# Kernel optimization log

Hardware: AMD Instinct MI355X
Metric: run time of the kernel (lower is better)

## Reference

```python
import jax, jax.numpy as jnp
import numpy as np

N = 4096   # n_roi
E = 131072 # edges (avg degree 32)
B = 64     # batch of subjects/windows sharing one connectome
K = 4      # Chebyshev order


def _cheb_params(key, cin, cout):
    kw, kb = jax.random.split(key)
    w = jax.random.normal(kw, (K, cin, cout), dtype=jnp.float32) / np.sqrt(K * cin)
    b = jax.random.normal(kb, (cout,), dtype=jnp.float32) * 0.01
    return w, b


def _lin_params(key, cin, cout):
    kw, kb = jax.random.split(key)
    w = jax.random.normal(kw, (cin, cout), dtype=jnp.float32) / np.sqrt(cin)
    b = jax.random.normal(kb, (cout,), dtype=jnp.float32) * 0.01
    return w, b


def setup_inputs() -> dict:
    key = jax.random.key(0)
    ks = jax.random.split(key, 12)
    x = jax.random.normal(ks[0], (B, N, 1), dtype=jnp.float32)
    src = jax.random.randint(ks[1], (E,), 0, N, dtype=jnp.int32)
    dst = jax.random.randint(ks[2], (E,), 0, N, dtype=jnp.int32)
    edge_weight = jax.random.uniform(ks[3], (E,), dtype=jnp.float32)
    w1, b1 = _cheb_params(ks[4], 1, 32)
    w2, b2 = _cheb_params(ks[5], 32, 32)
    w3, b3 = _cheb_params(ks[6], 32, 32)
    w4, b4 = _cheb_params(ks[7], 32, 32)
    w5, b5 = _cheb_params(ks[8], 32, 4)
    fw1, fb1 = _lin_params(ks[9], N * 4, 128)
    fw2, fb2 = _lin_params(ks[10], 128, 128)
    fw3, fb3 = _lin_params(ks[11], 128, 9)
    return dict(x=x, src=src, dst=dst, edge_weight=edge_weight,
                w1=w1, b1=b1, w2=w2, b2=b2, w3=w3, b3=b3,
                w4=w4, b4=b4, w5=w5, b5=b5,
                fw1=fw1, fb1=fb1, fw2=fw2, fb2=fb2, fw3=fw3, fb3=fb3)


def _norm_weights(src, dst, edge_weight):
    # PyG ChebConv default: sym normalization, lambda_max=2 ->
    # L_hat = -D^{-1/2} A D^{-1/2}, diagonal 2/lambda_max - 1 = 0 (self-loop skipped)
    deg = jax.ops.segment_sum(edge_weight, src, num_segments=N)
    dinv = jnp.where(deg > 0, jax.lax.rsqrt(jnp.maximum(deg, 1e-30)), 0.0)
    return -dinv[src] * edge_weight * dinv[dst]


def _propagate(z, src, dst, nw):
    # z: [B, N, C] -> L_hat @ z  via gather-multiply-scatter over edges
    msg = nw[None, :, None] * z[:, src, :]          # [B, E, C]
    msg = jnp.swapaxes(msg, 0, 1)                    # [E, B, C]
    agg = jax.ops.segment_sum(msg, dst, num_segments=N)  # [N, B, C]
    return jnp.swapaxes(agg, 0, 1)                   # [B, N, C]


def _cheb_conv(x, src, dst, nw, w, b):
    # x: [B,N,Cin], w: [K,Cin,Cout]
    tx0 = x
    out = jnp.einsum('bni,io->bno', tx0, w[0])
    tx1 = _propagate(tx0, src, dst, nw)
    out = out + jnp.einsum('bni,io->bno', tx1, w[1])
    for k in range(2, K):
        tx2 = 2.0 * _propagate(tx1, src, dst, nw) - tx0
        out = out + jnp.einsum('bni,io->bno', tx2, w[k])
        tx0, tx1 = tx1, tx2
    return out + b


def reference(x, src, dst, edge_weight, w1, b1, w2, b2, w3, b3, w4, b4, w5, b5,
              fw1, fb1, fw2, fb2, fw3, fb3):
    nw = _norm_weights(src, dst, edge_weight)
    h = jax.nn.relu(_cheb_conv(x, src, dst, nw, w1, b1))
    h = jax.nn.relu(_cheb_conv(h, src, dst, nw, w2, b2))
    h = jax.nn.relu(_cheb_conv(h, src, dst, nw, w3, b3))
    h = jax.nn.relu(_cheb_conv(h, src, dst, nw, w4, b4))
    h = jax.nn.relu(_cheb_conv(h, src, dst, nw, w5, b5))  # [B, N, 4]
    h = h.reshape(B, N * 4)
    # original has dropout (identity at eval) and NO relu between fc layers
    h = h @ fw1 + fb1
    h = h @ fw2 + fb2
    return h @ fw3 + fb3  # [B, 9]
```

## Files before the change

### kernel.cpp

```cpp
#include <hip/hip_runtime.h>
#include <cstdint>

#define NN 4096
#define EE 131072
#define BB 64
#define EPAD (EE + 8 * NN)

typedef float f4 __attribute__((ext_vector_type(4)));
typedef unsigned short ushort_t;
typedef unsigned int uint_t;

__device__ __forceinline__ f4 up4(uint2 u) {
    f4 r;
    r.x = __uint_as_float(u.x << 16);
    r.y = __uint_as_float(u.x & 0xffff0000u);
    r.z = __uint_as_float(u.y << 16);
    r.w = __uint_as_float(u.y & 0xffff0000u);
    return r;
}
__device__ __forceinline__ void up8(uint4 u, f4& lo, f4& hi) {
    lo.x = __uint_as_float(u.x << 16);
    lo.y = __uint_as_float(u.x & 0xffff0000u);
    lo.z = __uint_as_float(u.y << 16);
    lo.w = __uint_as_float(u.y & 0xffff0000u);
    hi.x = __uint_as_float(u.z << 16);
    hi.y = __uint_as_float(u.z & 0xffff0000u);
    hi.z = __uint_as_float(u.w << 16);
    hi.w = __uint_as_float(u.w & 0xffff0000u);
}
__device__ __forceinline__ uint_t bfpk(float a, float b) {
    uint_t xa = __float_as_uint(a); xa = (xa + 0x7fffu + ((xa >> 16) & 1u)) >> 16;
    uint_t xb = __float_as_uint(b); xb = (xb + 0x7fffu + ((xb >> 16) & 1u));
    return (xa & 0xffffu) | (xb & 0xffff0000u);
}

__global__ void k_deg_hist(const int* __restrict__ src, const int* __restrict__ dst,
                           const float* __restrict__ ew, float* __restrict__ deg,
                           int* __restrict__ cnt) {
    int e = blockIdx.x * blockDim.x + threadIdx.x;
    if (e >= EE) return;
    atomicAdd(&deg[src[e]], ew[e]);
    atomicAdd(&cnt[dst[e]], 1);
}

__global__ __launch_bounds__(1024) void k_scan(const int* __restrict__ cnt,
                                               int* __restrict__ rowptr,
                                               int* __restrict__ cursor) {
    __shared__ int s[1024];
    int tid = threadIdx.x;
    int p0 = (cnt[tid * 4 + 0] + 7) & ~7;
    int p1 = (cnt[tid * 4 + 1] + 7) & ~7;
    int p2 = (cnt[tid * 4 + 2] + 7) & ~7;
    int p3 = (cnt[tid * 4 + 3] + 7) & ~7;
    int sum = p0 + p1 + p2 + p3;
    s[tid] = sum;
    __syncthreads();
    for (int off = 1; off < 1024; off <<= 1) {
        int t = (tid >= off) ? s[tid - off] : 0;
        __syncthreads();
        s[tid] += t;
        __syncthreads();
    }
    int excl = s[tid] - sum;
    rowptr[tid * 4 + 0] = excl; cursor[tid * 4 + 0] = excl; excl += p0;
    rowptr[tid * 4 + 1] = excl; cursor[tid * 4 + 1] = excl; excl += p1;
    rowptr[tid * 4 + 2] = excl; cursor[tid * 4 + 2] = excl; excl += p2;
    rowptr[tid * 4 + 3] = excl; cursor[tid * 4 + 3] = excl; excl += p3;
    if (tid == 1023) rowptr[4096] = excl;
}

__global__ void k_fill(const int* __restrict__ src, const int* __restrict__ dst,
                       const float* __restrict__ ew, const float* __restrict__ deg,
                       int* __restrict__ cursor, int2* __restrict__ cv) {
    int e = blockIdx.x * blockDim.x + threadIdx.x;
    if (e >= EE) return;
    int s = src[e], d = dst[e];
    int pos = atomicAdd(&cursor[d], 1);
    float ds = deg[s], dd = deg[d];
    float is = ds > 0.f ? rsqrtf(fmaxf(ds, 1e-30f)) : 0.f;
    float id = dd > 0.f ? rsqrtf(fmaxf(dd, 1e-30f)) : 0.f;
    float v = -(is * ew[e] * id);
    cv[pos] = make_int2(s, __float_as_int(v));
}

__global__ __launch_bounds__(256) void k_transpose_x(const float* __restrict__ x,
                                                     float* __restrict__ X0) {
    __shared__ float s[64 * 65];
    int n0 = blockIdx.x * 64;
    for (int idx = threadIdx.x; idx < 4096; idx += 256) {
        int b = idx >> 6, nl = idx & 63;
        s[nl * 65 + b] = x[(size_t)b * NN + n0 + nl];
    }
    __syncthreads();
    for (int idx = threadIdx.x; idx < 4096; idx += 256) {
        int nl = idx >> 6, b = idx & 63;
        X0[(size_t)(n0 + nl) * 64 + b] = s[nl * 65 + b];
    }
}

__global__ __launch_bounds__(64) void k_spmm_narrow(const int* __restrict__ rowptr,
                                                    const int2* __restrict__ cv,
                                                    const float* __restrict__ Zin,
                                                    const float* __restrict__ Tprev,
                                                    float* __restrict__ Tout,
                                                    float alpha, int useprev) {
    int n = blockIdx.x;
    int lane = threadIdx.x;
    int start = rowptr[n], end = rowptr[n + 1];
    float acc = 0.f;
    for (int e = start; e < end; e += 8) {
        const int4* q = reinterpret_cast<const int4*>(cv + e);
        int4 a = q[0], b = q[1], c = q[2], d = q[3];
        float z0 = Zin[((size_t)a.x << 6) + lane];
        float z1 = Zin[((size_t)a.z << 6) + lane];
        float z2 = Zin[((size_t)b.x << 6) + lane];
        float z3 = Zin[((size_t)b.z << 6) + lane];
        float z4 = Zin[((size_t)c.x << 6) + lane];
        float z5 = Zin[((size_t)c.z << 6) + lane];
        float z6 = Zin[((size_t)d.x << 6) + lane];
        float z7 = Zin[((size_t)d.z << 6) + lane];
        acc += __int_as_float(a.y) * z0 + __int_as_float(a.w) * z1
             + __int_as_float(b.y) * z2 + __int_as_float(b.w) * z3
             + __int_as_float(c.y) * z4 + __int_as_float(c.w) * z5
             + __int_as_float(d.y) * z6 + __int_as_float(d.w) * z7;
    }
    size_t o = ((size_t)n << 6) + lane;
    float r = alpha * acc;
    if (useprev) r -= Tprev[o];
    Tout[o] = r;
}

__global__ __launch_bounds__(256) void k_expand1(const float* __restrict__ T0,
                                                 const float* __restrict__ T1,
                                                 const float* __restrict__ T2,
                                                 const float* __restrict__ T3,
                                                 const float* __restrict__ w1,
                                                 const float* __restrict__ b1,
                                                 ushort_t* __restrict__ H) {
    __shared__ float sT[4][64];
    __shared__ float sW[128];
    __shared__ float sB[32];
    int n = blockIdx.x, tid = threadIdx.x;
    {
        int k = tid >> 6, b = tid & 63;
        const float* Tk = (k == 0) ? T0 : (k == 1) ? T1 : (k == 2) ? T2 : T3;
        sT[k][b] = Tk[(size_t)n * 64 + b];
    }
    if (tid < 128) sW[tid] = w1[tid];
    if (tid < 32) sB[tid] = b1[tid];
    __syncthreads();
    int col0 = tid * 8;
    int b = tid >> 2;
    int co0 = col0 & 31;
    float t0 = sT[0][b], t1 = sT[1][b], t2 = sT[2][b], t3 = sT[3][b];
    float r[8];
#pragma unroll
    for (int j = 0; j < 8; ++j) {
        int co = co0 + j;
        float v = t0 * sW[co] + t1 * sW[32 + co] + t2 * sW[64 + co] + t3 * sW[96 + co] + sB[co];
        r[j] = v > 0.f ? v : 0.f;
    }
    uint4 st;
    st.x = bfpk(r[0], r[1]); st.y = bfpk(r[2], r[3]);
    st.z = bfpk(r[4], r[5]); st.w = bfpk(r[6], r[7]);
    *reinterpret_cast<uint4*>(H + (size_t)n * 2048 + col0) = st;
}

__global__ __launch_bounds__(256) void k_spmm_pure(const int* __restrict__ rowptr,
                                                   const int2* __restrict__ cv,
                                                   const ushort_t* __restrict__ Zg,
                                                   const ushort_t* __restrict__ Pown,
                                                   ushort_t* __restrict__ Tout) {
    int chunk = blockIdx.x & 3;
    int rowblk = blockIdx.x >> 2;
    int wave = threadIdx.x >> 6;
    int lane = threadIdx.x & 63;
    int n = rowblk * 4 + wave;
    int col0 = chunk * 512 + lane * 8;

    int start = rowptr[n], end = rowptr[n + 1];
    f4 aL0 = {0,0,0,0}, aH0 = {0,0,0,0}, aL1 = {0,0,0,0}, aH1 = {0,0,0,0};
    for (int e = start; e < end; e += 8) {
        const int4* q = reinterpret_cast<const int4*>(cv + e);
        int4 a = q[0], b = q[1], c = q[2], d = q[3];
        uint4 u0 = *reinterpret_cast<const uint4*>(Zg + (((size_t)a.x) << 11) + col0);
        uint4 u1 = *reinterpret_cast<const uint4*>(Zg + (((size_t)a.z) << 11) + col0);
        uint4 u2 = *reinterpret_cast<const uint4*>(Zg + (((size_t)b.x) << 11) + col0);
        uint4 u3 = *reinterpret_cast<const uint4*>(Zg + (((size_t)b.z) << 11) + col0);
        uint4 u4 = *reinterpret_cast<const uint4*>(Zg + (((size_t)c.x) << 11) + col0);
        uint4 u5 = *reinterpret_cast<const uint4*>(Zg + (((size_t)c.z) << 11) + col0);
        uint4 u6 = *reinterpret_cast<const uint4*>(Zg + (((size_t)d.x) << 11) + col0);
        uint4 u7 = *reinterpret_cast<const uint4*>(Zg + (((size_t)d.z) << 11) + col0);
        f4 lo, hi;
        up8(u0, lo, hi); aL0 += __int_as_float(a.y) * lo; aH0 += __int_as_float(a.y) * hi;
        up8(u1, lo, hi); aL1 += __int_as_float(a.w) * lo; aH1 += __int_as_float(a.w) * hi;
        up8(u2, lo, hi); aL0 += __int_as_float(b.y) * lo; aH0 += __int_as_float(b.y) * hi;
        up8(u3, lo, hi); aL1 += __int_as_float(b.w) * lo; aH1 += __int_as_float(b.w) * hi;
        up8(u4, lo, hi); aL0 += __int_as_float(c.y) * lo; aH0 += __int_as_float(c.y) * hi;
        up8(u5, lo, hi); aL1 += __int_as_float(c.w) * lo; aH1 += __int_as_float(c.w) * hi;
        up8(u6, lo, hi); aL0 += __int_as_float(d.y) * lo; aH0 += __int_as_float(d.y) * hi;
        up8(u7, lo, hi); aL1 += __int_as_float(d.w) * lo; aH1 += __int_as_float(d.w) * hi;
    }
    size_t o = (((size_t)n) << 11) + col0;
    f4 tL = aL0 + aL1, tH = aH0 + aH1;
    if (Pown) {
        uint4 pu = *reinterpret_cast<const uint4*>(Pown + o);
        f4 pL, pH;
        up8(pu, pL, pH);
        tL = 2.f * tL - pL;
        tH = 2.f * tH - pH;
    }
    uint4 st;
    st.x = bfpk(tL.x, tL.y); st.y = bfpk(tL.z, tL.w);
    st.z = bfpk(tH.x, tH.y); st.w = bfpk(tH.z, tH.w);
    *reinterpret_cast<uint4*>(Tout + o) = st;
}

template <int COUT, bool OUTBF>
__global__ __launch_bounds__(256, 4) void k_cheb_out(
    const int* __restrict__ rowptr, const int2* __restrict__ cv,
    const ushort_t* __restrict__ T2g,
    const ushort_t* __restrict__ T1,
    const ushort_t* __restrict__ H,
    const float* __restrict__ W,
    const float* __restrict__ bias,
    void* __restrict__ OUTv)
{
    __shared__ float sW[4 * 32 * COUT];
    __shared__ uint_t sPu[4][4][320];

    int chunk = blockIdx.x & 3;
    int rowblk = blockIdx.x >> 2;
    int wave = threadIdx.x >> 6;
    int lane = threadIdx.x & 63;
    int n = rowblk * 4 + wave;
    int col0 = chunk * 512 + lane * 8;
    int tid = threadIdx.x;

    for (int idx = tid; idx < 4 * 32 * COUT; idx += 256) sW[idx] = W[idx];

    int start = rowptr[n], end = rowptr[n + 1];
    f4 aL0 = {0,0,0,0}, aH0 = {0,0,0,0}, aL1 = {0,0,0,0}, aH1 = {0,0,0,0};
    for (int e = start; e < end; e += 8) {
        const int4* q = reinterpret_cast<const int4*>(cv + e);
        int4 a = q[0], b = q[1], c = q[2], d = q[3];
        uint4 u0 = *reinterpret_cast<const uint4*>(T2g + (((size_t)a.x) << 11) + col0);
        uint4 u1 = *reinterpret_cast<const uint4*>(T2g + (((size_t)a.z) << 11) + col0);
        uint4 u2 = *reinterpret_cast<const uint4*>(T2g + (((size_t)b.x) << 11) + col0);
        uint4 u3 = *reinterpret_cast<const uint4*>(T2g + (((size_t)b.z) << 11) + col0);
        uint4 u4 = *reinterpret_cast<const uint4*>(T2g + (((size_t)c.x) << 11) + col0);
        uint4 u5 = *reinterpret_cast<const uint4*>(T2g + (((size_t)c.z) << 11) + col0);
        uint4 u6 = *reinterpret_cast<const uint4*>(T2g + (((size_t)d.x) << 11) + col0);
        uint4 u7 = *reinterpret_cast<const uint4*>(T2g + (((size_t)d.z) << 11) + col0);
        f4 lo, hi;
        up8(u0, lo, hi); aL0 += __int_as_float(a.y) * lo; aH0 += __int_as_float(a.y) * hi;
        up8(u1, lo, hi); aL1 += __int_as_float(a.w) * lo; aH1 += __int_as_float(a.w) * hi;
        up8(u2, lo, hi); aL0 += __int_as_float(b.y) * lo; aH0 += __int_as_float(b.y) * hi;
        up8(u3, lo, hi); aL1 += __int_as_float(b.w) * lo; aH1 += __int_as_float(b.w) * hi;
        up8(u4, lo, hi); aL0 += __int_as_float(c.y) * lo; aH0 += __int_as_float(c.y) * hi;
        up8(u5, lo, hi); aL1 += __int_as_float(c.w) * lo; aH1 += __int_as_float(c.w) * hi;
        up8(u6, lo, hi); aL0 += __int_as_float(d.y) * lo; aH0 += __int_as_float(d.y) * hi;
        up8(u7, lo, hi); aL1 += __int_as_float(d.w) * lo; aH1 += __int_as_float(d.w) * hi;
    }
    size_t o = (((size_t)n) << 11) + col0;

    int g = lane >> 2, qd = lane & 3;
    int si = g * 20 + qd * 4;
    {
        uint4 pu = *reinterpret_cast<const uint4*>(T1 + o);
        f4 pL, pH;
        up8(pu, pL, pH);
        f4 tL = 2.f * (aL0 + aL1) - pL;
        f4 tH = 2.f * (aH0 + aH1) - pH;
        uint4 st;
        st.x = bfpk(tL.x, tL.y); st.y = bfpk(tL.z, tL.w);
        st.z = bfpk(tH.x, tH.y); st.w = bfpk(tH.z, tH.w);
        *reinterpret_cast<uint4*>(&sPu[wave][3][si]) = st;
        *reinterpret_cast<uint4*>(&sPu[wave][1][si]) = pu;
    }
    *reinterpret_cast<uint4*>(&sPu[wave][2][si]) =
        *reinterpret_cast<const uint4*>(T2g + o);
    *reinterpret_cast<uint4*>(&sPu[wave][0][si]) =
        *reinterpret_cast<const uint4*>(H + o);
    __syncthreads();

    if constexpr (COUT == 32) {
        int co0 = qd * 8;
        f4 oacc0 = {0,0,0,0}, oacc1 = {0,0,0,0};
#pragma unroll
        for (int u = 0; u < 16; ++u) {
#pragma unroll
            for (int p = 0; p < 4; ++p) {
                uint_t au = sPu[wave][p][g * 20 + u];
                float alo = __uint_as_float(au << 16);
                float ahi = __uint_as_float(au & 0xffff0000u);
                const float* wr0 = &sW[p * 1024 + (2 * u) * 32 + co0];
                const float* wr1 = &sW[p * 1024 + (2 * u + 1) * 32 + co0];
                oacc0 += alo * *reinterpret_cast<const f4*>(wr0);
                oacc1 += alo * *reinterpret_cast<const f4*>(wr0 + 4);
                oacc0 += ahi * *reinterpret_cast<const f4*>(wr1);
                oacc1 += ahi * *reinterpret_cast<const f4*>(wr1 + 4);
            }
        }
        f4 r0, r1;
        r0.x = oacc0.x + bias[co0 + 0]; r0.y = oacc0.y + bias[co0 + 1];
        r0.z = oacc0.z + bias[co0 + 2]; r0.w = oacc0.w + bias[co0 + 3];
        r1.x = oacc1.x + bias[co0 + 4]; r1.y = oacc1.y + bias[co0 + 5];
        r1.z = oacc1.z + bias[co0 + 6]; r1.w = oacc1.w + bias[co0 + 7];
        r0.x = r0.x > 0.f ? r0.x : 0.f; r0.y = r0.y > 0.f ? r0.y : 0.f;
        r0.z = r0.z > 0.f ? r0.z : 0.f; r0.w = r0.w > 0.f ? r0.w : 0.f;
        r1.x = r1.x > 0.f ? r1.x : 0.f; r1.y = r1.y > 0.f ? r1.y : 0.f;
        r1.z = r1.z > 0.f ? r1.z : 0.f; r1.w = r1.w > 0.f ? r1.w : 0.f;
        if constexpr (OUTBF) {
            uint4 st;
            st.x = bfpk(r0.x, r0.y); st.y = bfpk(r0.z, r0.w);
            st.z = bfpk(r1.x, r1.y); st.w = bfpk(r1.z, r1.w);
            *reinterpret_cast<uint4*>((ushort_t*)OUTv + o) = st;
        } else {
            float* po = (float*)OUTv + o;
            *reinterpret_cast<f4*>(po) = r0;
            *reinterpret_cast<f4*>(po + 4) = r1;
        }
    } else {
        int co = lane & 3;
        float o0 = 0.f;
#pragma unroll
        for (int u = 0; u < 16; ++u) {
#pragma unroll
            for (int p = 0; p < 4; ++p) {
                uint_t au = sPu[wave][p][g * 20 + u];
                float alo = __uint_as_float(au << 16);
                float ahi = __uint_as_float(au & 0xffff0000u);
                o0 += alo * sW[p * 128 + (2 * u) * 4 + co]
                    + ahi * sW[p * 128 + (2 * u + 1) * 4 + co];
            }
        }
        float r = o0 + bias[co];
        r = r > 0.f ? r : 0.f;
        ((float*)OUTv)[n * 256 + chunk * 64 + lane] = r;
    }
}

__global__ __launch_bounds__(256) void k_fc1(const float* __restrict__ H5,
                                             const float* __restrict__ fw1,
                                             float* __restrict__ fc1out) {
    __shared__ float hT[128 * 65];
    __shared__ float wS[32 * 128];
    int tid = threadIdx.x;
    int n0 = blockIdx.x * 32;
    for (int idx = tid; idx < 8192; idx += 256) {
        int n_l = idx >> 8;
        int rem = idx & 255;
        int b = rem >> 2, c = rem & 3;
        int kk = n_l * 4 + c;
        hT[kk * 65 + b] = H5[(size_t)(n0 + n_l) * 256 + rem];
    }
    float acc[8][4];
#pragma unroll
    for (int i = 0; i < 8; ++i)
#pragma unroll
        for (int j = 0; j < 4; ++j) acc[i][j] = 0.f;
    int bq = tid >> 5;
    int jq = tid & 31;
    for (int kb = 0; kb < 128; kb += 32) {
        __syncthreads();
        for (int idx = tid; idx < 4096; idx += 256) {
            int kl = idx >> 7, j = idx & 127;
            wS[idx] = fw1[(size_t)(n0 * 4 + kb + kl) * 128 + j];
        }
        __syncthreads();
        for (int kl = 0; kl < 32; ++kl) {
            int kk = kb + kl;
            float4 w = *reinterpret_cast<const float4*>(&wS[kl * 128 + jq * 4]);
#pragma unroll
            for (int bi = 0; bi < 8; ++bi) {
                float h = hT[kk * 65 + bq * 8 + bi];
                acc[bi][0] += h * w.x;
                acc[bi][1] += h * w.y;
                acc[bi][2] += h * w.z;
                acc[bi][3] += h * w.w;
            }
        }
    }
#pragma unroll
    for (int bi = 0; bi < 8; ++bi)
#pragma unroll
        for (int ji = 0; ji < 4; ++ji)
            atomicAdd(&fc1out[(bq * 8 + bi) * 128 + jq * 4 + ji], acc[bi][ji]);
}

__global__ __launch_bounds__(128) void k_fc23(const float* __restrict__ fc1out,
                                              const float* __restrict__ fb1,
                                              const float* __restrict__ fw2,
                                              const float* __restrict__ fb2,
                                              const float* __restrict__ fw3,
                                              const float* __restrict__ fb3,
                                              float* __restrict__ out) {
    int b = blockIdx.x;
    int j = threadIdx.x;
    __shared__ float r[128];
    __shared__ float s1[128];
    r[j] = fc1out[b * 128 + j] + fb1[j];
    __syncthreads();
    float acc = fb2[j];
    for (int i = 0; i < 128; ++i) acc += r[i] * fw2[i * 128 + j];
    s1[j] = acc;
    __syncthreads();
    if (j < 9) {
        float a2 = fb3[j];
        for (int i = 0; i < 128; ++i) a2 += s1[i] * fw3[i * 9 + j];
        out[b * 9 + j] = a2;
    }
}

extern "C" void kernel_launch(void* const* d_in, const int* in_sizes, int n_in,
                              void* d_out, int out_size, void* d_ws, size_t ws_size,
                              hipStream_t stream) {
    const float* x   = (const float*)d_in[0];
    const int*   src = (const int*)d_in[1];
    const int*   dst = (const int*)d_in[2];
    const float* ew  = (const float*)d_in[3];
    const float* w1  = (const float*)d_in[4];
    const float* b1  = (const float*)d_in[5];
    const float* w2  = (const float*)d_in[6];
    const float* b2  = (const float*)d_in[7];
    const float* w3  = (const float*)d_in[8];
    const float* b3  = (const float*)d_in[9];
    const float* w4  = (const float*)d_in[10];
    const float* b4  = (const float*)d_in[11];
    const float* w5  = (const float*)d_in[12];
    const float* b5  = (const float*)d_in[13];
    const float* fw1 = (const float*)d_in[14];
    const float* fb1 = (const float*)d_in[15];
    const float* fw2 = (const float*)d_in[16];
    const float* fb2 = (const float*)d_in[17];
    const float* fw3 = (const float*)d_in[18];
    const float* fb3 = (const float*)d_in[19];
    float* out = (float*)d_out;

    char* p = (char*)d_ws;
    const size_t XBYTES = (size_t)NN * 2048 * 2;
    ushort_t* X0 = (ushort_t*)(p + 0 * XBYTES);
    ushort_t* X1 = (ushort_t*)(p + 1 * XBYTES);
    ushort_t* X2 = (ushort_t*)(p + 2 * XBYTES);
    ushort_t* X3 = (ushort_t*)(p + 3 * XBYTES);
    size_t off = 4 * XBYTES;
    float* H5     = (float*)(p + off); off += (size_t)NN * 256 * 4;
    float* deg    = (float*)(p + off); off += (size_t)NN * 4;
    int*   cnt    = (int*)(p + off);   off += (size_t)NN * 4;
    int*   cursor = (int*)(p + off);   off += (size_t)NN * 4;
    int*   rowptr = (int*)(p + off);   off += (size_t)(NN + 4) * 4;
    int2*  cv     = (int2*)(p + off);  off += (size_t)EPAD * 8;
    float* fc1o   = (float*)(p + off); off += (size_t)BB * 128 * 4;
    float* xn0    = (float*)(p + off); off += (size_t)NN * 64 * 4;
    float* tn1    = (float*)(p + off); off += (size_t)NN * 64 * 4;
    float* tn2    = (float*)(p + off); off += (size_t)NN * 64 * 4;
    float* tn3    = (float*)(p + off); off += (size_t)NN * 64 * 4;
    if (off > ws_size) return;

    hipMemsetAsync(deg, 0, NN * 4, stream);
    hipMemsetAsync(cnt, 0, NN * 4, stream);
    hipMemsetAsync(cv, 0, (size_t)EPAD * 8, stream);
    hipMemsetAsync(fc1o, 0, BB * 128 * 4, stream);

    k_deg_hist<<<EE / 256, 256, 0, stream>>>(src, dst, ew, deg, cnt);
    k_scan<<<1, 1024, 0, stream>>>(cnt, rowptr, cursor);
    k_fill<<<EE / 256, 256, 0, stream>>>(src, dst, ew, deg, cursor, cv);
    k_transpose_x<<<NN / 64, 256, 0, stream>>>(x, xn0);

    k_spmm_narrow<<<NN, 64, 0, stream>>>(rowptr, cv, xn0, nullptr, tn1, 1.f, 0);
    k_spmm_narrow<<<NN, 64, 0, stream>>>(rowptr, cv, tn1, xn0, tn2, 2.f, 1);
    k_spmm_narrow<<<NN, 64, 0, stream>>>(rowptr, cv, tn2, tn1, tn3, 2.f, 1);
    k_expand1<<<NN, 256, 0, stream>>>(xn0, tn1, tn2, tn3, w1, b1, X3);

    const int GRID4 = (NN / 4) * 4;
    auto run32 = [&](const ushort_t* H, ushort_t* T1, ushort_t* T2, ushort_t* OUT,
                     const float* W, const float* B) {
        k_spmm_pure<<<GRID4, 256, 0, stream>>>(rowptr, cv, H, nullptr, T1);
        k_spmm_pure<<<GRID4, 256, 0, stream>>>(rowptr, cv, T1, H, T2);
        k_cheb_out<32, true><<<GRID4, 256, 0, stream>>>(rowptr, cv, T2, T1, H, W, B, OUT);
    };
    run32(X3, X0, X1, X2, w2, b2);
    run32(X2, X3, X0, X1, w3, b3);
    run32(X1, X2, X3, X0, w4, b4);

    k_spmm_pure<<<GRID4, 256, 0, stream>>>(rowptr, cv, X0, nullptr, X1);
    k_spmm_pure<<<GRID4, 256, 0, stream>>>(rowptr, cv, X1, X0, X2);
    k_cheb_out<4, false><<<GRID4, 256, 0, stream>>>(rowptr, cv, X2, X1, X0, w5, b5, H5);

    k_fc1<<<128, 256, 0, stream>>>(H5, fw1, fc1o);
    k_fc23<<<BB, 128, 0, stream>>>(fc1o, fb1, fw2, fb2, fw3, fb3, out);
}
```

Measured before the change: 644.1 us.

## Use bf16 MFMA for the Chebyshev output projection in cheb_out kernel

Replaces the scalar FP32 FMA loop that projects the four Chebyshev terms (128 inputs to 32 outputs per node/batch slice) with bf16 MFMA 16x16x32 instructions. The weights are converted to packed bf16 in shared memory in a transposed layout so they can serve as B fragments. Launch bounds are raised to 5 blocks per CU. The change drops weight precision to bf16 and writes the output as scattered 16-bit stores instead of vectorized ones. The COUT==32 path now always writes bf16, ignoring the OUTBF template flag.

```diff
diff --git a/kernel.cpp b/kernel.cpp
--- a/kernel.cpp
+++ b/kernel.cpp
@@ -7,17 +7,10 @@
 #define EPAD (EE + 8 * NN)
 
 typedef float f4 __attribute__((ext_vector_type(4)));
+typedef short bf16x8 __attribute__((ext_vector_type(8)));
 typedef unsigned short ushort_t;
 typedef unsigned int uint_t;
 
-__device__ __forceinline__ f4 up4(uint2 u) {
-    f4 r;
-    r.x = __uint_as_float(u.x << 16);
-    r.y = __uint_as_float(u.x & 0xffff0000u);
-    r.z = __uint_as_float(u.y << 16);
-    r.w = __uint_as_float(u.y & 0xffff0000u);
-    return r;
-}
 __device__ __forceinline__ void up8(uint4 u, f4& lo, f4& hi) {
     lo.x = __uint_as_float(u.x << 16);
     lo.y = __uint_as_float(u.x & 0xffff0000u);
@@ -32,6 +25,10 @@
     uint_t xa = __float_as_uint(a); xa = (xa + 0x7fffu + ((xa >> 16) & 1u)) >> 16;
     uint_t xb = __float_as_uint(b); xb = (xb + 0x7fffu + ((xb >> 16) & 1u));
     return (xa & 0xffffu) | (xb & 0xffff0000u);
+}
+__device__ __forceinline__ ushort_t bf1(float a) {
+    uint_t x = __float_as_uint(a);
+    return (ushort_t)((x + 0x7fffu + ((x >> 16) & 1u)) >> 16);
 }
 
 __global__ void k_deg_hist(const int* __restrict__ src, const int* __restrict__ dst,
@@ -217,7 +214,7 @@
 }
 
 template <int COUT, bool OUTBF>
-__global__ __launch_bounds__(256, 4) void k_cheb_out(
+__global__ __launch_bounds__(256, 5) void k_cheb_out(
     const int* __restrict__ rowptr, const int2* __restrict__ cv,
     const ushort_t* __restrict__ T2g,
     const ushort_t* __restrict__ T1,
@@ -226,8 +223,9 @@
     const float* __restrict__ bias,
     void* __restrict__ OUTv)
 {
-    __shared__ float sW[4 * 32 * COUT];
     __shared__ uint_t sPu[4][4][320];
+    __shared__ uint_t sWb[(COUT == 32) ? 2560 : 1];
+    __shared__ float  sWf[(COUT == 4) ? 512 : 1];
 
     int chunk = blockIdx.x & 3;
     int rowblk = blockIdx.x >> 2;
@@ -237,7 +235,16 @@
     int col0 = chunk * 512 + lane * 8;
     int tid = threadIdx.x;
 
-    for (int idx = tid; idx < 4 * 32 * COUT; idx += 256) sW[idx] = W[idx];
+    if constexpr (COUT == 32) {
+        for (int idx = tid; idx < 2048; idx += 256) {
+            int p = idx >> 9, rem = idx & 511;
+            int co = rem >> 4, u = rem & 15;
+            sWb[p * 640 + co * 20 + u] =
+                bfpk(W[p * 1024 + (2 * u) * 32 + co], W[p * 1024 + (2 * u + 1) * 32 + co]);
+        }
+    } else {
+        for (int idx = tid; idx < 4 * 32 * COUT; idx += 256) sWf[idx] = W[idx];
+    }
 
     int start = rowptr[n], end = rowptr[n + 1];
     f4 aL0 = {0,0,0,0}, aH0 = {0,0,0,0}, aL1 = {0,0,0,0}, aH1 = {0,0,0,0};
@@ -285,8 +292,34 @@
     __syncthreads();
 
     if constexpr (COUT == 32) {
-        int co0 = qd * 8;
-        f4 oacc0 = {0,0,0,0}, oacc1 = {0,0,0,0};
+        int mr = lane & 15;
+        int qk = lane >> 4;
+        f4 accA = {0,0,0,0}, accB = {0,0,0,0};
+#pragma unroll
+        for (int kk = 0; kk < 4; ++kk) {
+            bf16x8 af = *reinterpret_cast<const bf16x8*>(&sPu[wave][kk][mr * 20 + qk * 4]);
+            bf16x8 b0 = *reinterpret_cast<const bf16x8*>(&sWb[kk * 640 + mr * 20 + qk * 4]);
+            bf16x8 b1 = *reinterpret_cast<const bf16x8*>(&sWb[kk * 640 + (16 + mr) * 20 + qk * 4]);
+            accA = __builtin_amdgcn_mfma_f32_16x16x32_bf16(af, b0, accA, 0, 0, 0);
+            accB = __builtin_amdgcn_mfma_f32_16x16x32_bf16(af, b1, accB, 0, 0, 0);
+        }
+        int co = lane & 15;
+        float bA = bias[co], bB = bias[co + 16];
+        ushort_t* OB = (ushort_t*)OUTv;
+        size_t obase = (((size_t)n) << 11) + chunk * 512;
+#pragma unroll
+        for (int r = 0; r < 4; ++r) {
+            int gb = (lane >> 4) * 4 + r;
+            float vA = accA[r] + bA;
+            float vB = accB[r] + bB;
+            vA = vA > 0.f ? vA : 0.f;
+            vB = vB > 0.f ? vB : 0.f;
+            OB[obase + gb * 32 + co]      = bf1(vA);
+            OB[obase + gb * 32 + co + 16] = bf1(vB);
+        }
+    } else {
+        int co = lane & 3;
+        float o0 = 0.f;
 #pragma unroll
         for (int u = 0; u < 16; ++u) {
 #pragma unroll
@@ -294,45 +327,8 @@
                 uint_t au = sPu[wave][p][g * 20 + u];
                 float alo = __uint_as_float(au << 16);
                 float ahi = __uint_as_float(au & 0xffff0000u);
-                const float* wr0 = &sW[p * 1024 + (2 * u) * 32 + co0];
-                const float* wr1 = &sW[p * 1024 + (2 * u + 1) * 32 + co0];
-                oacc0 += alo * *reinterpret_cast<const f4*>(wr0);
-                oacc1 += alo * *reinterpret_cast<const f4*>(wr0 + 4);
-                oacc0 += ahi * *reinterpret_cast<const f4*>(wr1);
-                oacc1 += ahi * *reinterpret_cast<const f4*>(wr1 + 4);
-            }
-        }
-        f4 r0, r1;
-        r0.x = oacc0.x + bias[co0 + 0]; r0.y = oacc0.y + bias[co0 + 1];
-        r0.z = oacc0.z + bias[co0 + 2]; r0.w = oacc0.w + bias[co0 + 3];
-        r1.x = oacc1.x + bias[co0 + 4]; r1.y = oacc1.y + bias[co0 + 5];
-        r1.z = oacc1.z + bias[co0 + 6]; r1.w = oacc1.w + bias[co0 + 7];
-        r0.x = r0.x > 0.f ? r0.x : 0.f; r0.y = r0.y > 0.f ? r0.y : 0.f;
-        r0.z = r0.z > 0.f ? r0.z : 0.f; r0.w = r0.w > 0.f ? r0.w : 0.f;
-        r1.x = r1.x > 0.f ? r1.x : 0.f; r1.y = r1.y > 0.f ? r1.y : 0.f;
-        r1.z = r1.z > 0.f ? r1.z : 0.f; r1.w = r1.w > 0.f ? r1.w : 0.f;
-        if constexpr (OUTBF) {
-            uint4 st;
-            st.x = bfpk(r0.x, r0.y); st.y = bfpk(r0.z, r0.w);
-            st.z = bfpk(r1.x, r1.y); st.w = bfpk(r1.z, r1.w);
-            *reinterpret_cast<uint4*>((ushort_t*)OUTv + o) = st;
-        } else {
-            float* po = (float*)OUTv + o;
-            *reinterpret_cast<f4*>(po) = r0;
-            *reinterpret_cast<f4*>(po + 4) = r1;
-        }
-    } else {
-        int co = lane & 3;
-        float o0 = 0.f;
-#pragma unroll
-        for (int u = 0; u < 16; ++u) {
-#pragma unroll
-            for (int p = 0; p < 4; ++p) {
-                uint_t au = sPu[wave][p][g * 20 + u];
-                float alo = __uint_as_float(au << 16);
-                float ahi = __uint_as_float(au & 0xffff0000u);
-                o0 += alo * sW[p * 128 + (2 * u) * 4 + co]
-                    + ahi * sW[p * 128 + (2 * u + 1) * 4 + co];
+                o0 += alo * sWf[p * 128 + (2 * u) * 4 + co]
+                    + ahi * sWf[p * 128 + (2 * u + 1) * 4 + co];
             }
         }
         float r = o0 + bias[co];
```

Result: no change. 640.5 us (median of 2 runs) (-0.6%).
